# Kernel tuning notes

Hardware: AMD Instinct MI355X
Metric: run time of the kernel (lower is better)

Reference implementation:

```python
import jax, jax.numpy as jnp
import numpy as np

D_MODEL = 1024
N_HEADS = 16
HEAD_DIM = D_MODEL // N_HEADS


def setup_inputs() -> dict:
    key = jax.random.key(0)
    k1, k2, k3 = jax.random.split(key, 3)
    x = jax.random.normal(k1, (8, 1024, D_MODEL), dtype=jnp.float32)
    qkv_w = jax.random.normal(k2, (3 * D_MODEL, D_MODEL), dtype=jnp.float32) * 0.02
    qkv_b = jnp.zeros((3 * D_MODEL,), dtype=jnp.float32)
    proj_w = jax.random.normal(k3, (D_MODEL, D_MODEL), dtype=jnp.float32) * 0.02
    proj_b = jnp.zeros((D_MODEL,), dtype=jnp.float32)
    return {"x": x, "qkv_w": qkv_w, "qkv_b": qkv_b, "proj_w": proj_w, "proj_b": proj_b}


def reference(x, qkv_w, qkv_b, proj_w, proj_b):
    B, N, C = x.shape
    H, Dh = N_HEADS, HEAD_DIM
    # fused QKV projection (torch Linear: x @ W^T + b)
    qkv = x @ qkv_w.T + qkv_b                      # [B, N, 3C]
    qkv = qkv.reshape(B, N, 3, H, Dh).transpose(2, 0, 3, 1, 4)  # [3, B, H, N, Dh]
    q, k, v = qkv[0], qkv[1], qkv[2]
    scale = Dh ** -0.5
    attn = jnp.einsum("bhnd,bhmd->bhnm", q, k) * scale  # [B, H, N, N]
    attn = jax.nn.softmax(attn, axis=-1)
    out = jnp.einsum("bhnm,bhmd->bhnd", attn, v)        # [B, H, N, Dh]
    out = out.transpose(0, 2, 1, 3).reshape(B, N, C)
    return out @ proj_w.T + proj_b
```

## Files before the change

kernel.cpp:

```cpp
#include <hip/hip_runtime.h>
#include <hip/hip_bf16.h>
#include <stdint.h>

#define D_MODEL 1024
#define NHEADS  16
#define HDIM    64
#define SEQ     1024
#define BATCH   8

typedef __bf16 bf16;
typedef bf16  bf16x8 __attribute__((ext_vector_type(8)));
typedef float f32x4  __attribute__((ext_vector_type(4)));
typedef uint32_t u32;

__device__ __forceinline__ int swzi(int row, int col) {
    return (row << 6) + (col ^ ((row & 7) << 3));
}

__device__ __forceinline__ void gload_lds16(const bf16* g, bf16* l) {
    __builtin_amdgcn_global_load_lds(
        (const __attribute__((address_space(1))) void*)g,
        (__attribute__((address_space(3))) void*)l, 16, 0, 0);
}

__global__ void cvt_kernel(const float* __restrict__ in, bf16* __restrict__ out, int n) {
    int i = (blockIdx.x * 256 + threadIdx.x) * 8;
    if (i >= n) return;
    float4 a = *reinterpret_cast<const float4*>(in + i);
    float4 b = *reinterpret_cast<const float4*>(in + i + 4);
    union { bf16 h[8]; uint4 u; } pk;
    pk.h[0] = (bf16)a.x; pk.h[1] = (bf16)a.y; pk.h[2] = (bf16)a.z; pk.h[3] = (bf16)a.w;
    pk.h[4] = (bf16)b.x; pk.h[5] = (bf16)b.y; pk.h[6] = (bf16)b.z; pk.h[7] = (bf16)b.w;
    *reinterpret_cast<uint4*>(out + i) = pk.u;
}

__device__ __forceinline__ void gemm_tile_acc(
    const bf16* __restrict__ A, const bf16* __restrict__ B, int K,
    int m0, int n0, bf16* As, bf16* Bs,
    f32x4 acc[4][4], int wr, int wc, int lane, int tid)
{
    for (int kt = 0; kt < K; kt += 64) {
        __syncthreads();
#pragma unroll
        for (int c = 0; c < 4; ++c) {
            int chunk = tid + c * 256;
            int r   = chunk >> 3;
            int j   = chunk & 7;
            int jg  = j ^ (r & 7);
            gload_lds16(A + (size_t)(m0 + r) * K + kt + jg * 8, As + chunk * 8);
            gload_lds16(B + (size_t)(n0 + r) * K + kt + jg * 8, Bs + chunk * 8);
        }
        __syncthreads();
#pragma unroll
        for (int kk = 0; kk < 2; ++kk) {
            bf16x8 af[4], bfr[4];
#pragma unroll
            for (int t = 0; t < 4; ++t) {
                af[t]  = *reinterpret_cast<const bf16x8*>(As + swzi(wr * 64 + t * 16 + (lane & 15), kk * 32 + ((lane >> 4) << 3)));
                bfr[t] = *reinterpret_cast<const bf16x8*>(Bs + swzi(wc * 64 + t * 16 + (lane & 15), kk * 32 + ((lane >> 4) << 3)));
            }
#pragma unroll
            for (int i = 0; i < 4; ++i)
#pragma unroll
                for (int j2 = 0; j2 < 4; ++j2)
                    acc[i][j2] = __builtin_amdgcn_mfma_f32_16x16x32_bf16(af[i], bfr[j2], acc[i][j2], 0, 0, 0);
        }
    }
}

__global__ __launch_bounds__(256)
void qkv_gemm(const bf16* __restrict__ X, const bf16* __restrict__ W,
              const float* __restrict__ bias,
              bf16* __restrict__ q_ws, bf16* __restrict__ k_ws, bf16* __restrict__ vt_ws)
{
    __shared__ __align__(16) bf16 As[128 * 64];
    __shared__ __align__(16) bf16 Bs[128 * 64];
    const int NB = 3072 / 128;
    int bm = blockIdx.x / NB, bn = blockIdx.x % NB;
    int m0 = bm * 128, n0 = bn * 128;
    int tid = threadIdx.x, lane = tid & 63, w = tid >> 6;
    int wr = w >> 1, wc = w & 1;
    f32x4 acc[4][4];
#pragma unroll
    for (int i = 0; i < 4; ++i)
#pragma unroll
        for (int j = 0; j < 4; ++j) acc[i][j] = (f32x4){0.f, 0.f, 0.f, 0.f};

    gemm_tile_acc(X, W, 1024, m0, n0, As, Bs, acc, wr, wc, lane, tid);

#pragma unroll
    for (int i = 0; i < 4; ++i) {
        int mbase = m0 + wr * 64 + i * 16 + ((lane >> 4) << 2);
#pragma unroll
        for (int j = 0; j < 4; ++j) {
            int col = n0 + wc * 64 + j * 16 + (lane & 15);
            int which = col >> 10, rem = col & 1023;
            int h = rem >> 6, d = rem & 63;
            float bi = bias[col];
            int b = mbase >> 10, nrow0 = mbase & 1023;
            int bh = b * NHEADS + h;
            if (which == 2) {
                union { bf16 h4[4]; uint2 u; } vp;
#pragma unroll
                for (int r = 0; r < 4; ++r) vp.h4[r] = (bf16)(acc[i][j][r] + bi);
                *reinterpret_cast<uint2*>(vt_ws + ((size_t)bh * HDIM + d) * SEQ + nrow0) = vp.u;
            } else {
                bf16* dst = (which == 0) ? q_ws : k_ws;
                float scl = (which == 0) ? 0.125f : 1.0f;
#pragma unroll
                for (int r = 0; r < 4; ++r) {
                    float v = (acc[i][j][r] + bi) * scl;
                    dst[((size_t)bh * SEQ + nrow0 + r) * HDIM + d] = (bf16)v;
                }
            }
        }
    }
}

__global__ __launch_bounds__(256)
void proj_gemm(const bf16* __restrict__ Ao, const bf16* __restrict__ W,
               const float* __restrict__ bias, float* __restrict__ out)
{
    __shared__ __align__(16) bf16 As[128 * 64];
    __shared__ __align__(16) bf16 Bs[128 * 64];
    const int NB = 1024 / 128;
    int bm = blockIdx.x / NB, bn = blockIdx.x % NB;
    int m0 = bm * 128, n0 = bn * 128;
    int tid = threadIdx.x, lane = tid & 63, w = tid >> 6;
    int wr = w >> 1, wc = w & 1;
    f32x4 acc[4][4];
#pragma unroll
    for (int i = 0; i < 4; ++i)
#pragma unroll
        for (int j = 0; j < 4; ++j) acc[i][j] = (f32x4){0.f, 0.f, 0.f, 0.f};

    gemm_tile_acc(Ao, W, 1024, m0, n0, As, Bs, acc, wr, wc, lane, tid);

#pragma unroll
    for (int i = 0; i < 4; ++i) {
        int mbase = m0 + wr * 64 + i * 16 + ((lane >> 4) << 2);
#pragma unroll
        for (int j = 0; j < 4; ++j) {
            int col = n0 + wc * 64 + j * 16 + (lane & 15);
            float bi = bias[col];
#pragma unroll
            for (int r = 0; r < 4; ++r)
                out[(size_t)(mbase + r) * D_MODEL + col] = acc[i][j][r] + bi;
        }
    }
}

__global__ __launch_bounds__(256)
void attn_kernel(const bf16* __restrict__ Q, const bf16* __restrict__ K,
                 const bf16* __restrict__ Vt, bf16* __restrict__ AO)
{
    __shared__ __align__(16) bf16 kl[64 * 64];
    __shared__ __align__(16) bf16 vl[64 * 64];
    int bh = blockIdx.x & 127;
    int qt = blockIdx.x >> 7;
    int tid = threadIdx.x, lane = tid & 63, w = tid >> 6;
    int g = lane >> 4, q = lane & 15;
    const bf16* Qb  = Q  + (size_t)bh * SEQ * HDIM;
    const bf16* Kb  = K  + (size_t)bh * SEQ * HDIM;
    const bf16* Vtb = Vt + (size_t)bh * HDIM * SEQ;

    int qrow = qt * 64 + w * 16 + q;
    bf16x8 qf[2];
#pragma unroll
    for (int kk = 0; kk < 2; ++kk)
        qf[kk] = *reinterpret_cast<const bf16x8*>(Qb + (size_t)qrow * HDIM + kk * 32 + (g << 3));

    f32x4 o[4];
#pragma unroll
    for (int dt = 0; dt < 4; ++dt) o[dt] = (f32x4){0.f, 0.f, 0.f, 0.f};
    float plsumA = 0.f, plsumB = 0.f;

    int srcA = ((g & 1) << 5) + q;
    int srcB = srcA + 16;
    bool hi = (g >> 1) != 0;

    const bf16* ksrc[2]; const bf16* vsrc[2]; bf16* kdst[2]; bf16* vdst[2];
#pragma unroll
    for (int c = 0; c < 2; ++c) {
        int chunk = tid + c * 256;
        int r  = chunk >> 3;
        int j  = chunk & 7;
        int jg = j ^ (r & 7);
        ksrc[c] = Kb  + (size_t)r * HDIM + jg * 8;
        vsrc[c] = Vtb + (size_t)r * SEQ + jg * 8;
        kdst[c] = kl + chunk * 8;
        vdst[c] = vl + chunk * 8;
    }

    for (int t = 0; t < 16; ++t) {
        __syncthreads();
#pragma unroll
        for (int c = 0; c < 2; ++c) {
            gload_lds16(ksrc[c], kdst[c]);
            gload_lds16(vsrc[c], vdst[c]);
            ksrc[c] += 64 * HDIM;
            vsrc[c] += 64;
        }
        __syncthreads();

        f32x4 s[4];
#pragma unroll
        for (int nt = 0; nt < 4; ++nt) {
            s[nt] = (f32x4){0.f, 0.f, 0.f, 0.f};
#pragma unroll
            for (int kk = 0; kk < 2; ++kk) {
                bf16x8 kf = *reinterpret_cast<const bf16x8*>(
                    kl + swzi(nt * 16 + q, kk * 32 + (g << 3)));
                s[nt] = __builtin_amdgcn_mfma_f32_16x16x32_bf16(kf, qf[kk], s[nt], 0, 0, 0);
            }
        }

        u32 pkk[4][2];
#pragma unroll
        for (int nt = 0; nt < 4; ++nt)
#pragma unroll
            for (int half = 0; half < 2; ++half) {
                float pa = __expf(s[nt][2 * half]     - 4.0f);
                float pb = __expf(s[nt][2 * half + 1] - 4.0f);
                if (half == 0) plsumA += pa + pb; else plsumB += pa + pb;
                union { bf16 h[2]; u32 u; } pw;
                pw.h[0] = (bf16)pa; pw.h[1] = (bf16)pb;
                pkk[nt][half] = pw.u;
            }

#pragma unroll
        for (int ks = 0; ks < 2; ++ks) {
            union { u32 u[4]; bf16x8 v; } pb;
            u32 a0 = __shfl((int)pkk[2 * ks][0],     srcA);
            u32 a1 = __shfl((int)pkk[2 * ks + 1][0], srcA);
            pb.u[0] = hi ? a1 : a0;
            u32 b0 = __shfl((int)pkk[2 * ks][1],     srcA);
            u32 b1 = __shfl((int)pkk[2 * ks + 1][1], srcA);
            pb.u[1] = hi ? b1 : b0;
            u32 c0 = __shfl((int)pkk[2 * ks][0],     srcB);
            u32 c1 = __shfl((int)pkk[2 * ks + 1][0], srcB);
            pb.u[2] = hi ? c1 : c0;
            u32 d0 = __shfl((int)pkk[2 * ks][1],     srcB);
            u32 d1 = __shfl((int)pkk[2 * ks + 1][1], srcB);
            pb.u[3] = hi ? d1 : d0;
#pragma unroll
            for (int dt = 0; dt < 4; ++dt) {
                bf16x8 vfr = *reinterpret_cast<const bf16x8*>(
                    vl + swzi(dt * 16 + q, ks * 32 + (g << 3)));
                o[dt] = __builtin_amdgcn_mfma_f32_16x16x32_bf16(vfr, pb.v, o[dt], 0, 0, 0);
            }
        }
    }

    float plsum = plsumA + plsumB;
    plsum += __shfl_xor(plsum, 16);
    plsum += __shfl_xor(plsum, 32);
    float inv = 1.f / plsum;

    int b = bh >> 4, h = bh & 15;
    size_t base = ((size_t)b * SEQ + qrow) * D_MODEL + h * HDIM;
#pragma unroll
    for (int dt = 0; dt < 4; ++dt) {
        union { bf16 h4[4]; uint2 u; } ob;
#pragma unroll
        for (int r = 0; r < 4; ++r) ob.h4[r] = (bf16)(o[dt][r] * inv);
        *reinterpret_cast<uint2*>(AO + base + dt * 16 + (g << 2)) = ob.u;
    }
}

extern "C" void kernel_launch(void* const* d_in, const int* in_sizes, int n_in,
                              void* d_out, int out_size, void* d_ws, size_t ws_size,
                              hipStream_t stream) {
    const float* x      = (const float*)d_in[0];
    const float* qkv_w  = (const float*)d_in[1];
    const float* qkv_b  = (const float*)d_in[2];
    const float* proj_w = (const float*)d_in[3];
    const float* proj_b = (const float*)d_in[4];
    float* out = (float*)d_out;
    char* ws = (char*)d_ws;

    bf16* x_bf    = (bf16*)(ws);
    bf16* wqkv_bf = (bf16*)(ws + (size_t)(16 << 20));
    bf16* wproj_bf= (bf16*)(ws + (size_t)(22 << 20));
    bf16* q_ws    = (bf16*)(ws + (size_t)(24 << 20));
    bf16* k_ws    = (bf16*)(ws + (size_t)(40 << 20));
    bf16* vt_ws   = (bf16*)(ws + (size_t)(56 << 20));
    bf16* ao_ws   = x_bf;

    cvt_kernel<<<(8192 * 1024) / 2048, 256, 0, stream>>>(x, x_bf, 8192 * 1024);
    cvt_kernel<<<(3072 * 1024) / 2048, 256, 0, stream>>>(qkv_w, wqkv_bf, 3072 * 1024);
    cvt_kernel<<<(1024 * 1024) / 2048, 256, 0, stream>>>(proj_w, wproj_bf, 1024 * 1024);

    qkv_gemm<<<64 * 24, 256, 0, stream>>>(x_bf, wqkv_bf, qkv_b, q_ws, k_ws, vt_ws);
    attn_kernel<<<128 * 16, 256, 0, stream>>>(q_ws, k_ws, vt_ws, ao_ws);
    proj_gemm<<<64 * 8, 256, 0, stream>>>(ao_ws, wproj_bf, proj_b, out);
}
```

Measured before the change: 178.6 us.

## Merge conversion launches and double attention KV tile to 128 keys

The three fp32-to-bf16 conversion launches become one kernel that picks its source buffer by index range, which removes two launches. The attention kernel now stages 128 keys per iteration instead of 64, halving the number of loop iterations and barrier pairs. The V-transpose tile gets a new 16-way XOR swizzle to fit the wider rows. The trade-off is doubled shared memory per block, which may lower occupancy.

```diff
diff --git a/kernel.cpp b/kernel.cpp
--- a/kernel.cpp
+++ b/kernel.cpp
@@ -23,15 +23,21 @@
         (__attribute__((address_space(3))) void*)l, 16, 0, 0);
 }
 
-__global__ void cvt_kernel(const float* __restrict__ in, bf16* __restrict__ out, int n) {
+__global__ void cvt3_kernel(const float* __restrict__ x,  bf16* __restrict__ ox, int nx,
+                            const float* __restrict__ w1, bf16* __restrict__ o1, int n1,
+                            const float* __restrict__ w2, bf16* __restrict__ o2, int n2) {
     int i = (blockIdx.x * 256 + threadIdx.x) * 8;
-    if (i >= n) return;
-    float4 a = *reinterpret_cast<const float4*>(in + i);
-    float4 b = *reinterpret_cast<const float4*>(in + i + 4);
+    const float* src; bf16* dst;
+    if (i < nx)           { src = x  + i;            dst = ox + i; }
+    else if (i < nx + n1) { src = w1 + (i - nx);     dst = o1 + (i - nx); }
+    else if (i < nx + n1 + n2) { src = w2 + (i - nx - n1); dst = o2 + (i - nx - n1); }
+    else return;
+    float4 a = *reinterpret_cast<const float4*>(src);
+    float4 b = *reinterpret_cast<const float4*>(src + 4);
     union { bf16 h[8]; uint4 u; } pk;
     pk.h[0] = (bf16)a.x; pk.h[1] = (bf16)a.y; pk.h[2] = (bf16)a.z; pk.h[3] = (bf16)a.w;
     pk.h[4] = (bf16)b.x; pk.h[5] = (bf16)b.y; pk.h[6] = (bf16)b.z; pk.h[7] = (bf16)b.w;
-    *reinterpret_cast<uint4*>(out + i) = pk.u;
+    *reinterpret_cast<uint4*>(dst) = pk.u;
 }
 
 __device__ __forceinline__ void gemm_tile_acc(
@@ -154,8 +160,8 @@
 void attn_kernel(const bf16* __restrict__ Q, const bf16* __restrict__ K,
                  const bf16* __restrict__ Vt, bf16* __restrict__ AO)
 {
-    __shared__ __align__(16) bf16 kl[64 * 64];
-    __shared__ __align__(16) bf16 vl[64 * 64];
+    __shared__ __align__(16) bf16 kl[128 * 64];
+    __shared__ __align__(16) bf16 vl[64 * 128];
     int bh = blockIdx.x & 127;
     int qt = blockIdx.x >> 7;
     int tid = threadIdx.x, lane = tid & 63, w = tid >> 6;
@@ -179,75 +185,82 @@
     int srcB = srcA + 16;
     bool hi = (g >> 1) != 0;
 
-    const bf16* ksrc[2]; const bf16* vsrc[2]; bf16* kdst[2]; bf16* vdst[2];
-#pragma unroll
-    for (int c = 0; c < 2; ++c) {
-        int chunk = tid + c * 256;
-        int r  = chunk >> 3;
-        int j  = chunk & 7;
+    const bf16* ksrc[4]; const bf16* vsrc[4]; bf16* kdst[4]; bf16* vdst[4];
+#pragma unroll
+    for (int c = 0; c < 4; ++c) {
+        int ch = tid + c * 256;
+        int r  = ch >> 3;
+        int j  = ch & 7;
         int jg = j ^ (r & 7);
-        ksrc[c] = Kb  + (size_t)r * HDIM + jg * 8;
-        vsrc[c] = Vtb + (size_t)r * SEQ + jg * 8;
-        kdst[c] = kl + chunk * 8;
-        vdst[c] = vl + chunk * 8;
-    }
-
-    for (int t = 0; t < 16; ++t) {
+        ksrc[c] = Kb + (size_t)r * HDIM + jg * 8;
+        kdst[c] = kl + ch * 8;
+        int d   = ch >> 4;
+        int jn  = ch & 15;
+        int jng = jn ^ (d & 15);
+        vsrc[c] = Vtb + (size_t)d * SEQ + jng * 8;
+        vdst[c] = vl + ch * 8;
+    }
+
+    for (int t = 0; t < 8; ++t) {
         __syncthreads();
 #pragma unroll
-        for (int c = 0; c < 2; ++c) {
+        for (int c = 0; c < 4; ++c) {
             gload_lds16(ksrc[c], kdst[c]);
             gload_lds16(vsrc[c], vdst[c]);
-            ksrc[c] += 64 * HDIM;
-            vsrc[c] += 64;
+            ksrc[c] += 128 * HDIM;
+            vsrc[c] += 128;
         }
         __syncthreads();
 
-        f32x4 s[4];
-#pragma unroll
-        for (int nt = 0; nt < 4; ++nt) {
-            s[nt] = (f32x4){0.f, 0.f, 0.f, 0.f};
-#pragma unroll
-            for (int kk = 0; kk < 2; ++kk) {
-                bf16x8 kf = *reinterpret_cast<const bf16x8*>(
-                    kl + swzi(nt * 16 + q, kk * 32 + (g << 3)));
-                s[nt] = __builtin_amdgcn_mfma_f32_16x16x32_bf16(kf, qf[kk], s[nt], 0, 0, 0);
+#pragma unroll
+        for (int h = 0; h < 2; ++h) {
+            f32x4 s[4];
+#pragma unroll
+            for (int nt = 0; nt < 4; ++nt) {
+                s[nt] = (f32x4){0.f, 0.f, 0.f, 0.f};
+#pragma unroll
+                for (int kk = 0; kk < 2; ++kk) {
+                    bf16x8 kf = *reinterpret_cast<const bf16x8*>(
+                        kl + swzi(h * 64 + nt * 16 + q, kk * 32 + (g << 3)));
+                    s[nt] = __builtin_amdgcn_mfma_f32_16x16x32_bf16(kf, qf[kk], s[nt], 0, 0, 0);
+                }
             }
-        }
-
-        u32 pkk[4][2];
-#pragma unroll
-        for (int nt = 0; nt < 4; ++nt)
-#pragma unroll
-            for (int half = 0; half < 2; ++half) {
-                float pa = __expf(s[nt][2 * half]     - 4.0f);
-                float pb = __expf(s[nt][2 * half + 1] - 4.0f);
-                if (half == 0) plsumA += pa + pb; else plsumB += pa + pb;
-                union { bf16 h[2]; u32 u; } pw;
-                pw.h[0] = (bf16)pa; pw.h[1] = (bf16)pb;
-                pkk[nt][half] = pw.u;
-            }
-
-#pragma unroll
-        for (int ks = 0; ks < 2; ++ks) {
-            union { u32 u[4]; bf16x8 v; } pb;
-            u32 a0 = __shfl((int)pkk[2 * ks][0],     srcA);
-            u32 a1 = __shfl((int)pkk[2 * ks + 1][0], srcA);
-            pb.u[0] = hi ? a1 : a0;
-            u32 b0 = __shfl((int)pkk[2 * ks][1],     srcA);
-            u32 b1 = __shfl((int)pkk[2 * ks + 1][1], srcA);
-            pb.u[1] = hi ? b1 : b0;
-            u32 c0 = __shfl((int)pkk[2 * ks][0],     srcB);
-            u32 c1 = __shfl((int)pkk[2 * ks + 1][0], srcB);
-            pb.u[2] = hi ? c1 : c0;
-            u32 d0 = __shfl((int)pkk[2 * ks][1],     srcB);
-            u32 d1 = __shfl((int)pkk[2 * ks + 1][1], srcB);
-            pb.u[3] = hi ? d1 : d0;
-#pragma unroll
-            for (int dt = 0; dt < 4; ++dt) {
-                bf16x8 vfr = *reinterpret_cast<const bf16x8*>(
-                    vl + swzi(dt * 16 + q, ks * 32 + (g << 3)));
-                o[dt] = __builtin_amdgcn_mfma_f32_16x16x32_bf16(vfr, pb.v, o[dt], 0, 0, 0);
+
+            u32 pkk[4][2];
+#pragma unroll
+            for (int nt = 0; nt < 4; ++nt)
+#pragma unroll
+                for (int half = 0; half < 2; ++half) {
+                    float pa = __expf(s[nt][2 * half]     - 4.0f);
+                    float pb = __expf(s[nt][2 * half + 1] - 4.0f);
+                    if (half == 0) plsumA += pa + pb; else plsumB += pa + pb;
+                    union { bf16 hh[2]; u32 u; } pw;
+                    pw.hh[0] = (bf16)pa; pw.hh[1] = (bf16)pb;
+                    pkk[nt][half] = pw.u;
+                }
+
+#pragma unroll
+            for (int ks = 0; ks < 2; ++ks) {
+                union { u32 u[4]; bf16x8 v; } pb;
+                u32 a0 = __shfl((int)pkk[2 * ks][0],     srcA);
+                u32 a1 = __shfl((int)pkk[2 * ks + 1][0], srcA);
+                pb.u[0] = hi ? a1 : a0;
+                u32 b0 = __shfl((int)pkk[2 * ks][1],     srcA);
+                u32 b1 = __shfl((int)pkk[2 * ks + 1][1], srcA);
+                pb.u[1] = hi ? b1 : b0;
+                u32 c0 = __shfl((int)pkk[2 * ks][0],     srcB);
+                u32 c1 = __shfl((int)pkk[2 * ks + 1][0], srcB);
+                pb.u[2] = hi ? c1 : c0;
+                u32 d0 = __shfl((int)pkk[2 * ks][1],     srcB);
+                u32 d1 = __shfl((int)pkk[2 * ks + 1][1], srcB);
+                pb.u[3] = hi ? d1 : d0;
+#pragma unroll
+                for (int dt = 0; dt < 4; ++dt) {
+                    int d = dt * 16 + q;
+                    int ch = (8 * h + 4 * ks + g) ^ q;
+                    bf16x8 vfr = *reinterpret_cast<const bf16x8*>(vl + d * 128 + ch * 8);
+                    o[dt] = __builtin_amdgcn_mfma_f32_16x16x32_bf16(vfr, pb.v, o[dt], 0, 0, 0);
+                }
             }
         }
     }
@@ -287,9 +300,9 @@
     bf16* vt_ws   = (bf16*)(ws + (size_t)(56 << 20));
     bf16* ao_ws   = x_bf;
 
-    cvt_kernel<<<(8192 * 1024) / 2048, 256, 0, stream>>>(x, x_bf, 8192 * 1024);
-    cvt_kernel<<<(3072 * 1024) / 2048, 256, 0, stream>>>(qkv_w, wqkv_bf, 3072 * 1024);
-    cvt_kernel<<<(1024 * 1024) / 2048, 256, 0, stream>>>(proj_w, wproj_bf, 1024 * 1024);
+    const int NX = 8192 * 1024, N1 = 3072 * 1024, N2 = 1024 * 1024;
+    cvt3_kernel<<<(NX + N1 + N2) / 2048, 256, 0, stream>>>(
+        x, x_bf, NX, qkv_w, wqkv_bf, N1, proj_w, wproj_bf, N2);
 
     qkv_gemm<<<64 * 24, 256, 0, stream>>>(x_bf, wqkv_bf, qkv_b, q_ws, k_ws, vt_ws);
     attn_kernel<<<128 * 16, 256, 0, stream>>>(q_ws, k_ws, vt_ws, ao_ws);
```

New measurement: 176.1 us. About the same (-1.4%).
